# Optimization experiments

Hardware: AMD Instinct MI355X
Metric: run time of the kernel (lower is better)

The kernel has to match this reference:

```python
import jax, jax.numpy as jnp
import numpy as np

TEMP = 0.1
EDGE_THR = 0.25
PATCH = 16
SAMPLE = 100
EPS = 1e-12


def _split_into_patches(feats, P):
    # replicates torch unfold(2).unfold(3).unfold(4).contiguous().view(B,-1,C,P,P,P)
    B, C, D, H, W = feats.shape
    x = feats.reshape(B, C, D // P, P, H // P, P, W // P, P)
    x = x.transpose(0, 1, 2, 4, 6, 3, 5, 7)  # [B,C,Dp,Hp,Wp,P,P,P]
    return x.reshape(B, -1, C, P, P, P)       # C-order reshape == torch .view on contiguous


def _projector(x, w1, b1, w2, b2):
    # torch Linear: y = x @ W.T + b
    h = jax.nn.relu(jnp.matmul(x, w1.T) + b1)
    return jnp.matmul(h, w2.T) + b2


def _normalize(x, axis):
    n = jnp.sqrt(jnp.sum(x * x, axis=axis, keepdims=True))
    return x / jnp.maximum(n, EPS)


def _conv3d(x, w, b, padding):
    y = jax.lax.conv_general_dilated(
        x, w, window_strides=(1, 1, 1), padding=padding,
        dimension_numbers=('NCDHW', 'OIDHW', 'NCDHW'))
    return y + b[None, :, None, None, None]


def setup_inputs() -> dict:
    key = jax.random.key(0)
    ks = jax.random.split(key, 12)
    B, C, D, H, W = 2, 128, 64, 64, 64
    inp = {
        'anchor_feats': jax.random.normal(ks[0], (B, C, D, H, W), dtype=jnp.float32),
        'positive_feats': jax.random.normal(ks[1], (B, C, D, H, W), dtype=jnp.float32),
        'conv1_w': jax.random.normal(ks[2], (32, C, 3, 3, 3), dtype=jnp.float32) * 0.02,
        'conv1_b': jnp.zeros((32,), dtype=jnp.float32),
        'conv2_w': jax.random.normal(ks[3], (1, 32, 1, 1, 1), dtype=jnp.float32) * 0.1,
        'conv2_b': jnp.zeros((1,), dtype=jnp.float32),
        'proj_w1': jax.random.normal(ks[4], (C, C), dtype=jnp.float32) * (1.0 / np.sqrt(C)),
        'proj_b1': jnp.zeros((C,), dtype=jnp.float32),
        'proj_w2': jax.random.normal(ks[5], (64, C), dtype=jnp.float32) * (1.0 / np.sqrt(C)),
        'proj_b2': jnp.zeros((64,), dtype=jnp.float32),
        'loss_weights': jnp.array([1.0, 0.7], dtype=jnp.float32),
        'voxel_idx': jax.random.permutation(ks[6], PATCH ** 3)[:SAMPLE].astype(jnp.int64),
    }
    return inp


def reference(anchor_feats, positive_feats, conv1_w, conv1_b, conv2_w, conv2_b,
              proj_w1, proj_b1, proj_w2, proj_b2, loss_weights, voxel_idx):
    B, C, D, H, W = anchor_feats.shape
    P = PATCH

    # region classifier: Conv3d(C,32,3,p=1) -> ReLU -> Conv3d(32,1,1) -> Sigmoid
    h = jax.nn.relu(_conv3d(anchor_feats, conv1_w, conv1_b, ((1, 1), (1, 1), (1, 1))))
    region_probs = jax.nn.sigmoid(_conv3d(h, conv2_w, conv2_b, ((0, 0), (0, 0), (0, 0))))
    region_mask = (region_probs > EDGE_THR).astype(jnp.float32)  # [B,1,D,H,W]

    anchor_p = _split_into_patches(anchor_feats, P)    # [B,N,C,P,P,P]
    positive_p = _split_into_patches(positive_feats, P)
    region_p = _split_into_patches(region_mask, P)     # [B,N,1,P,P,P]

    edge_ratio = jnp.mean(region_p, axis=(2, 3, 4, 5))  # [B,N]
    mask_vox = (edge_ratio > 0.6).astype(jnp.float32)
    mask_patch = (edge_ratio < 0.4).astype(jnp.float32)

    # ---- patch-level contrast (vectorized over B,N) ----
    a_vec = jnp.mean(anchor_p, axis=(3, 4, 5))    # [B,N,C]
    p_vec = jnp.mean(positive_p, axis=(3, 4, 5))
    a_proj = _normalize(_projector(a_vec, proj_w1, proj_b1, proj_w2, proj_b2), -1)
    p_proj = _normalize(_projector(p_vec, proj_w1, proj_b1, proj_w2, proj_b2), -1)
    patch_losses = -jnp.sum(a_proj * p_proj, axis=-1) / TEMP  # [B,N]

    # ---- voxel-level contrast (vectorized over B,N) ----
    N = anchor_p.shape[1]
    a_vox = anchor_p.reshape(B, N, C, P ** 3).transpose(0, 1, 3, 2)[:, :, voxel_idx, :]  # [B,N,S,C]
    p_vox = positive_p.reshape(B, N, C, P ** 3).transpose(0, 1, 3, 2)[:, :, voxel_idx, :]
    a_vp = _normalize(_projector(a_vox, proj_w1, proj_b1, proj_w2, proj_b2), -1)  # [B,N,S,64]
    p_vp = _normalize(_projector(p_vox, proj_w1, proj_b1, proj_w2, proj_b2), -1)
    sim = jnp.einsum('bnsd,bntd->bnst', a_vp, p_vp) / TEMP  # [B,N,S,S]
    lse = jax.nn.logsumexp(sim, axis=-1)                    # [B,N,S]
    diag = jnp.diagonal(sim, axis1=-2, axis2=-1)            # [B,N,S]
    vox_losses = jnp.mean(lse - diag, axis=-1)              # [B,N]

    patch_sum = jnp.sum(patch_losses * mask_patch)
    vox_sum = jnp.sum(vox_losses * mask_vox)
    valid = jnp.sum(mask_patch) + jnp.sum(mask_vox)

    total = (loss_weights[0] * patch_sum + loss_weights[1] * vox_sum)
    return jnp.where(valid > 0, total / jnp.maximum(valid, 1.0), 0.0)
```

## Files before the change

### kernel.cpp

```cpp
#include <hip/hip_runtime.h>

using short8 = __attribute__((ext_vector_type(8))) short;
using f32x16 = __attribute__((ext_vector_type(16))) float;

#define THR_LOGIT (-1.0986122886681098f)
#define ZPAGE_OFF 156509184

__device__ __forceinline__ unsigned short f2bf(float f) {
  unsigned u = __float_as_uint(f);
  u = (u + 0x7FFFu + ((u >> 16) & 1u)) >> 16;
  return (unsigned short)u;
}

__device__ __forceinline__ void async_copy16(void* lds, const void* g) {
  __builtin_amdgcn_global_load_lds(
      (const __attribute__((address_space(1))) unsigned int*)g,
      (__attribute__((address_space(3))) unsigned int*)lds, 16, 0, 0);
}

__global__ void __launch_bounds__(256) k_prep(const float* __restrict__ c1w,
    const float* __restrict__ pw1, const float* __restrict__ pw2,
    short* __restrict__ wt2, float* __restrict__ w1t, float* __restrict__ w2t) {
  int i = blockIdx.x * 256 + threadIdx.x;
  if (i < 110592) {
    int j8 = i & 7, l31v = (i >> 3) & 31, halfv = (i >> 8) & 1;
    int q = i >> 9;
    int dz = q % 3; q /= 3;
    int dx = q % 3; q /= 3;
    int dy = q % 3; int co8 = q / 3;
    int c = co8 * 16 + halfv * 8 + j8;
    int tap = dz * 9 + dy * 3 + dx;
    wt2[i] = (short)f2bf(c1w[l31v * 3456 + c * 27 + tap]);
  } else if (i < 126976) {
    int i2 = i - 110592; int c = i2 >> 7; int j = i2 & 127;
    w1t[i2] = pw1[j * 128 + c];
  } else if (i < 135168) {
    int i3 = i - 126976; int j = i3 >> 6; int d = i3 & 63;
    w2t[i3] = pw2[d * 128 + j];
  }
}

__global__ void k_inv(const int* __restrict__ vidx, int* __restrict__ inv) {
  int t = threadIdx.x;
  for (int k = t; k < 4096; k += 256) inv[k] = -1;
  __syncthreads();
  if (t < 100) inv[vidx[t]] = t;
}

__global__ void __launch_bounds__(256) k_stage(const float* __restrict__ src,
    short* __restrict__ in2, float* __restrict__ S4, float* __restrict__ Xmat,
    const int* __restrict__ inv, int vox_row_base) {
  __shared__ float tile[128][65];
  __shared__ int mcnt;
  __shared__ int mx[64];
  __shared__ int mrow[64];
  int bi = blockIdx.x;
  int b = bi >> 8, z = (bi >> 2) & 63, yp = bi & 3;
  int t = threadIdx.x;
  int zp = z >> 4, pz = z & 15;
  int cc = t & 127, xh = t >> 7;
  float part0 = 0.f, part1 = 0.f;

  for (int y0 = 0; y0 < 16; ++y0) {
    int y = yp * 16 + y0;
    __syncthreads();
    if (t == 0) mcnt = 0;
    {
      int xq = (t & 15) * 4, w = t >> 4;
      const float* sp = src + (long)b * 128 * 262144 + (long)z * 4096 + (long)y * 64 + xq;
      #pragma unroll
      for (int s = 0; s < 8; ++s) {
        int c = s * 16 + w;
        float4 v = *(const float4*)(sp + (long)c * 262144);
        tile[c][xq + 0] = v.x;
        tile[c][xq + 1] = v.y;
        tile[c][xq + 2] = v.z;
        tile[c][xq + 3] = v.w;
      }
    }
    __syncthreads();
    if (in2 != nullptr) {
      long rowbase = ((long)(b * 64 + z) * 64 + y) * 8192;
      int x = t >> 2, q = t & 3;
      int slot = (q & 1) ^ ((x >> 2) & 1);
      #pragma unroll
      for (int i = 0; i < 4; ++i) {
        int co8 = i * 2 + (q >> 1);
        short8 pk;
        #pragma unroll
        for (int j = 0; j < 8; ++j) pk[j] = (short)f2bf(tile[i * 32 + q * 8 + j][x]);
        *(short8*)(in2 + rowbase + co8 * 1024 + x * 16 + slot * 8) = pk;
      }
    }
    {
      float s0 = 0.f, s1 = 0.f;
      #pragma unroll
      for (int px = 0; px < 16; ++px) s0 += tile[cc][(xh * 2) * 16 + px];
      #pragma unroll
      for (int px = 0; px < 16; ++px) s1 += tile[cc][(xh * 2 + 1) * 16 + px];
      part0 += s0; part1 += s1;
    }
    if (t < 64) {
      int s = inv[pz * 256 + y0 * 16 + (t & 15)];
      if (s >= 0) {
        int idx = atomicAdd(&mcnt, 1);
        mx[idx] = t;
        int n = zp * 16 + yp * 4 + (t >> 4);
        mrow[idx] = vox_row_base + (b * 64 + n) * 100 + s;
      }
    }
    __syncthreads();
    int mc = mcnt;
    for (int i = 0; i < mc; ++i) {
      if (t < 128) Xmat[(long)mrow[i] * 128 + t] = tile[t][mx[i]];
    }
  }
  long sb = ((long)(b * 64 + z) * 4 + yp) * 512;
  S4[sb + cc * 4 + xh * 2 + 0] = part0;
  S4[sb + cc * 4 + xh * 2 + 1] = part1;
}

__global__ void __launch_bounds__(256, 2) k_conv(const short* __restrict__ in2,
    const short* __restrict__ wt2, const float* __restrict__ c1b,
    const float* __restrict__ c2w, const float* __restrict__ c2b,
    int* __restrict__ counts) {
  extern __shared__ char smem[];
  __shared__ int lcnt[4];
  int bi0 = blockIdx.x;
  int bi = ((bi0 & 7) << 7) | (bi0 >> 3);
  int b = bi >> 9, zb = (bi >> 4) & 31, yg = bi & 15;
  int z0 = zb * 2, y0 = yg * 4;
  int tid = threadIdx.x;
  int lane = tid & 63;
  int l31 = lane & 31, half = lane >> 5;
  int wave = tid >> 6;
  int xh = wave & 1, yo = wave >> 1;

  if (tid < 4) lcnt[tid] = 0;
  *(int*)(smem + 49152 + tid * 4) = 0;
  int zoff = 49152 + lane * 16;

  int gbase[12];
  int gmask[12];
  #pragma unroll
  for (int k = 0; k < 12; ++k) {
    int g = k * 256 + tid;
    int row = g >> 7, pos = g & 127;
    int zz = z0 - 1 + row / 6;
    int yy = y0 - 1 + row % 6;
    bool v = ((unsigned)zz < 64u) && ((unsigned)yy < 64u);
    gbase[k] = v ? (((b * 64 + zz) * 64 + yy) * 16384 + pos * 16)
                 : (ZPAGE_OFF + pos * 16);
    gmask[k] = v ? -1 : 0;
  }
  const char* gsrc = (const char*)in2;

  int xbase = xh * 32 + l31;
  int offA[3];
  int vmA[3];
  #pragma unroll
  for (int d = 0; d < 3; ++d) {
    int xp = xbase + d - 1;
    bool v = (unsigned)xp < 64u;
    int xc = min(max(xp, 0), 63);
    offA[d] = v ? (xc * 32 + ((half ^ ((xc >> 2) & 1)) << 4)) : zoff;
    vmA[d] = v ? -1 : 0;
  }
  int ybase = yo * 4096;
  const short8* pBbase = (const short8*)wt2 + half * 32 + l31;

  f32x16 acc[2][2] = {};

  #pragma unroll
  for (int k = 0; k < 12; ++k)
    async_copy16(smem + (k * 256 + tid) * 16, gsrc + gbase[k]);
  __syncthreads();

  for (int co8 = 0; co8 < 8; ++co8) {
    #pragma unroll
    for (int dx = 0; dx < 3; ++dx) {
      int m = vmA[dx], o = offA[dx];
      short8 A[4][4];
      #pragma unroll
      for (int zs = 0; zs < 4; ++zs)
        #pragma unroll
        for (int yr = 0; yr < 4; ++yr)
          A[zs][yr] = *(const short8*)(smem +
              (((zs * 12288 + yr * 2048) + ybase) & m) + o);
      __builtin_amdgcn_s_setprio(1);
      #pragma unroll
      for (int dz = 0; dz < 3; ++dz) {
        #pragma unroll
        for (int dy = 0; dy < 3; ++dy) {
          short8 bf = pBbase[((co8 * 9 + dy * 3 + dx) * 3 + dz) * 64];
          acc[0][0] = __builtin_amdgcn_mfma_f32_32x32x16_bf16(A[dz + 0][dy + 0], bf, acc[0][0], 0, 0, 0);
          acc[1][0] = __builtin_amdgcn_mfma_f32_32x32x16_bf16(A[dz + 1][dy + 0], bf, acc[1][0], 0, 0, 0);
          acc[0][1] = __builtin_amdgcn_mfma_f32_32x32x16_bf16(A[dz + 0][dy + 1], bf, acc[0][1], 0, 0, 0);
          acc[1][1] = __builtin_amdgcn_mfma_f32_32x32x16_bf16(A[dz + 1][dy + 1], bf, acc[1][1], 0, 0, 0);
        }
      }
      __builtin_amdgcn_s_setprio(0);
    }
    __syncthreads();
    if (co8 < 7) {
      int cadd = (co8 + 1) * 2048;
      #pragma unroll
      for (int k = 0; k < 12; ++k)
        async_copy16(smem + (k * 256 + tid) * 16,
                     gsrc + gbase[k] + (cadd & gmask[k]));
      __syncthreads();
    }
  }

  float b1v = c1b[l31];
  float w2v = c2w[l31];
  float b2v = c2b[0];
  int cnt0 = 0, cnt1 = 0;
  #pragma unroll
  for (int zi = 0; zi < 2; ++zi) {
    #pragma unroll
    for (int yi = 0; yi < 2; ++yi) {
      #pragma unroll
      for (int r = 0; r < 16; ++r) {
        float v = fmaxf(acc[zi][yi][r] + b1v, 0.f) * w2v;
        v += __shfl_xor(v, 1);
        v += __shfl_xor(v, 2);
        v += __shfl_xor(v, 4);
        v += __shfl_xor(v, 8);
        v += __shfl_xor(v, 16);
        int bit = (v + b2v) > THR_LOGIT;
        if (r < 8) cnt0 += bit; else cnt1 += bit;
      }
    }
  }
  if (l31 == 0) {
    atomicAdd(&lcnt[xh * 2 + 0], cnt0);
    atomicAdd(&lcnt[xh * 2 + 1], cnt1);
  }
  __syncthreads();
  if (tid < 4) {
    int n = (zb >> 3) * 16 + (yg >> 2) * 4 + tid;
    atomicAdd(&counts[b * 64 + n], lcnt[tid]);
  }
}

__global__ void __launch_bounds__(256) k_vecreduce(const float* __restrict__ S4a,
    const float* __restrict__ S4p, float* __restrict__ Xmat) {
  int g = blockIdx.x * 256 + threadIdx.x;
  int ten = g >> 14, rem = g & 16383;
  int b = rem >> 13, n = (rem >> 7) & 63, c = rem & 127;
  int zp = n >> 4, yp = (n >> 2) & 3, xp = n & 3;
  const float* S = ten ? S4p : S4a;
  float s = 0.f;
  #pragma unroll
  for (int k = 0; k < 16; ++k)
    s += S[((long)(b * 64 + zp * 16 + k) * 4 + yp) * 512 + c * 4 + xp];
  Xmat[(long)(ten * 128 + b * 64 + n) * 128 + c] = s * (1.f / 4096.f);
}

__global__ void __launch_bounds__(256) k_proj(const float* __restrict__ Xmat,
    const float* __restrict__ w1t, const float* __restrict__ pb1,
    const float* __restrict__ w2t, const float* __restrict__ pb2,
    float* __restrict__ P) {
  __shared__ float xsT[128][20];
  __shared__ float hsT[128][20];
  __shared__ float os[16][68];
  int bi = blockIdx.x;
  long row0 = (long)bi * 16;
  int t = threadIdx.x;
  {
    int r = t >> 4, c0 = (t & 15) * 8;
    const float* xp = Xmat + (row0 + r) * 128 + c0;
    #pragma unroll
    for (int k = 0; k < 8; ++k) xsT[c0 + k][r] = xp[k];
  }
  __syncthreads();
  {
    int j = t & 127, rh = t >> 7;
    float hacc[8];
    float bb = pb1[j];
    #pragma unroll
    for (int r8 = 0; r8 < 8; ++r8) hacc[r8] = bb;
    for (int c = 0; c < 128; ++c) {
      float w = w1t[c * 128 + j];
      float4 xlo = *(const float4*)&xsT[c][rh * 8];
      float4 xhi = *(const float4*)&xsT[c][rh * 8 + 4];
      hacc[0] += xlo.x * w; hacc[1] += xlo.y * w; hacc[2] += xlo.z * w; hacc[3] += xlo.w * w;
      hacc[4] += xhi.x * w; hacc[5] += xhi.y * w; hacc[6] += xhi.z * w; hacc[7] += xhi.w * w;
    }
    #pragma unroll
    for (int r8 = 0; r8 < 8; ++r8) hsT[j][rh * 8 + r8] = fmaxf(hacc[r8], 0.f);
  }
  __syncthreads();
  {
    int d = t & 63, rq = t >> 6;
    float oacc[4];
    float bb = pb2[d];
    #pragma unroll
    for (int r4 = 0; r4 < 4; ++r4) oacc[r4] = bb;
    for (int j = 0; j < 128; ++j) {
      float w = w2t[j * 64 + d];
      float4 hv = *(const float4*)&hsT[j][rq * 4];
      oacc[0] += hv.x * w; oacc[1] += hv.y * w; oacc[2] += hv.z * w; oacc[3] += hv.w * w;
    }
    #pragma unroll
    for (int r4 = 0; r4 < 4; ++r4) os[rq * 4 + r4][d] = oacc[r4];
  }
  __syncthreads();
  {
    int r = t >> 4, dg = t & 15;
    float4 v = *(const float4*)&os[r][dg * 4];
    float ss = v.x * v.x + v.y * v.y + v.z * v.z + v.w * v.w;
    ss += __shfl_xor(ss, 1); ss += __shfl_xor(ss, 2);
    ss += __shfl_xor(ss, 4); ss += __shfl_xor(ss, 8);
    float sc = 1.f / fmaxf(sqrtf(ss), 1e-12f);
    float4 o; o.x = v.x * sc; o.y = v.y * sc; o.z = v.z * sc; o.w = v.w * sc;
    *(float4*)&P[(row0 + r) * 64 + dg * 4] = o;
  }
}

__global__ void __launch_bounds__(128) k_sim(const float* __restrict__ P,
                                             float* __restrict__ vloss) {
  __shared__ float ps[100][68];
  __shared__ float red[128];
  int bn = blockIdx.x;
  int t = threadIdx.x;
  long pbase = (long)(13056 + bn * 100) * 64;
  for (int i = t; i < 1600; i += 128) {
    int r = i >> 4, dg = i & 15;
    *(float4*)&ps[r][dg * 4] = *(const float4*)&P[pbase + r * 64 + dg * 4];
  }
  float4 areg[16];
  long abase = (long)(256 + bn * 100) * 64;
  if (t < 100) {
    #pragma unroll
    for (int j = 0; j < 16; ++j) areg[j] = *(const float4*)&P[abase + (long)t * 64 + j * 4];
  }
  __syncthreads();
  float res = 0.f;
  if (t < 100) {
    float m = -1e30f, sum = 0.f, diag = 0.f;
    for (int t2 = 0; t2 < 100; ++t2) {
      float d = 0.f;
      #pragma unroll
      for (int j = 0; j < 16; ++j) {
        float4 pv = *(const float4*)&ps[t2][j * 4];
        d += areg[j].x * pv.x + areg[j].y * pv.y + areg[j].z * pv.z + areg[j].w * pv.w;
      }
      float sim = d * 10.f;
      if (t2 == t) diag = sim;
      float nm = fmaxf(m, sim);
      sum = sum * __expf(m - nm) + __expf(sim - nm);
      m = nm;
    }
    res = m + logf(sum) - diag;
  }
  red[t] = res;
  __syncthreads();
  if (t == 0) {
    float s = 0.f;
    for (int i = 0; i < 100; ++i) s += red[i];
    vloss[bn] = s * 0.01f;
  }
}

__global__ void __launch_bounds__(128) k_final(const float* __restrict__ P,
    const float* __restrict__ vloss, const int* __restrict__ counts,
    const float* __restrict__ lw, float* __restrict__ out) {
  int t = threadIdx.x;
  int lane = t & 63;
  float pterm = 0.f, vterm = 0.f; int vcnt = 0;
  {
    int c = counts[t];
    bool maskv = c >= 2458;
    bool maskp = c <= 1638;
    float d = 0.f;
    for (int k = 0; k < 64; ++k) d += P[t * 64 + k] * P[(128 + t) * 64 + k];
    if (maskp) { pterm = -d * 10.f; vcnt += 1; }
    if (maskv) { vterm = vloss[t];  vcnt += 1; }
  }
  for (int m = 1; m < 64; m <<= 1) {
    pterm += __shfl_xor(pterm, m);
    vterm += __shfl_xor(vterm, m);
    vcnt  += __shfl_xor(vcnt, m);
  }
  __shared__ float sp[2], sv[2]; __shared__ int sc[2];
  if (lane == 0) { sp[t >> 6] = pterm; sv[t >> 6] = vterm; sc[t >> 6] = vcnt; }
  __syncthreads();
  if (t == 0) {
    float psum = sp[0] + sp[1], vsum = sv[0] + sv[1];
    int vc = sc[0] + sc[1];
    float total = lw[0] * psum + lw[1] * vsum;
    out[0] = (vc > 0) ? total / (float)vc : 0.f;
  }
}

extern "C" void kernel_launch(void* const* d_in, const int* in_sizes, int n_in,
                              void* d_out, int out_size, void* d_ws, size_t ws_size,
                              hipStream_t stream) {
  const float* anchor   = (const float*)d_in[0];
  const float* positive = (const float*)d_in[1];
  const float* c1w = (const float*)d_in[2];
  const float* c1b = (const float*)d_in[3];
  const float* c2w = (const float*)d_in[4];
  const float* c2b = (const float*)d_in[5];
  const float* pw1 = (const float*)d_in[6];
  const float* pb1 = (const float*)d_in[7];
  const float* pw2 = (const float*)d_in[8];
  const float* pb2 = (const float*)d_in[9];
  const float* lw  = (const float*)d_in[10];
  const int*   vidx = (const int*)d_in[11];

  char* ws = (char*)d_ws;
  short* in2   = (short*)(ws + 0);
  float* S4a   = (float*)(ws + 134217728);
  float* S4p   = (float*)(ws + 135266304);
  float* X     = (float*)(ws + 136314880);
  float* P     = (float*)(ws + 149553152);
  short* wt2   = (short*)(ws + 156172288);
  float* w1t   = (float*)(ws + 156393472);
  float* w2t   = (float*)(ws + 156459008);
  int*   inv   = (int*)  (ws + 156491776);
  int*   counts= (int*)  (ws + 156508160);
  float* vloss = (float*)(ws + 156508672);
  short* zpage = (short*)(ws + ZPAGE_OFF);

  hipFuncSetAttribute(reinterpret_cast<const void*>(k_conv),
                      hipFuncAttributeMaxDynamicSharedMemorySize, 50176);

  hipMemsetAsync(counts, 0, 128 * sizeof(int), stream);
  hipMemsetAsync(zpage, 0, 16384, stream);
  k_prep<<<528, 256, 0, stream>>>(c1w, pw1, pw2, wt2, w1t, w2t);
  k_inv<<<1, 256, 0, stream>>>(vidx, inv);
  k_stage<<<512, 256, 0, stream>>>(anchor,   in2,     S4a, X, inv, 256);
  k_stage<<<512, 256, 0, stream>>>(positive, nullptr, S4p, X, inv, 13056);
  k_conv<<<1024, 256, 50176, stream>>>(in2, wt2, c1b, c2w, c2b, counts);
  k_vecreduce<<<128, 256, 0, stream>>>(S4a, S4p, X);
  k_proj<<<1616, 256, 0, stream>>>(X, w1t, pb1, w2t, pb2, P);
  k_sim<<<128, 128, 0, stream>>>(P, vloss);
  k_final<<<1, 128, 0, stream>>>(P, vloss, counts, lw, (float*)d_out);
}
```

Before: 415.2 us.

## Fuse positive-feature staging into conv kernel as interleaved block role

```diff
diff --git a/kernel.cpp b/kernel.cpp
--- a/kernel.cpp
+++ b/kernel.cpp
@@ -47,6 +47,74 @@
   if (t < 100) inv[vidx[t]] = t;
 }
 
+__device__ __forceinline__ void stage_body(float (*tile)[65], int* mcnt_p, int* mx,
+    int* mrow, int bi, int t, const float* __restrict__ src, short* __restrict__ in2,
+    float* __restrict__ S4, float* __restrict__ Xmat, const int* __restrict__ inv,
+    int vox_row_base) {
+  int b = bi >> 8, z = (bi >> 2) & 63, yp = bi & 3;
+  int zp = z >> 4, pz = z & 15;
+  int cc = t & 127, xh = t >> 7;
+  float part0 = 0.f, part1 = 0.f;
+
+  for (int y0 = 0; y0 < 16; ++y0) {
+    int y = yp * 16 + y0;
+    __syncthreads();
+    if (t == 0) *mcnt_p = 0;
+    {
+      int xq = (t & 15) * 4, w = t >> 4;
+      const float* sp = src + (long)b * 128 * 262144 + (long)z * 4096 + (long)y * 64 + xq;
+      #pragma unroll
+      for (int s = 0; s < 8; ++s) {
+        int c = s * 16 + w;
+        float4 v = *(const float4*)(sp + (long)c * 262144);
+        tile[c][xq + 0] = v.x;
+        tile[c][xq + 1] = v.y;
+        tile[c][xq + 2] = v.z;
+        tile[c][xq + 3] = v.w;
+      }
+    }
+    __syncthreads();
+    if (in2 != nullptr) {
+      long rowbase = ((long)(b * 64 + z) * 64 + y) * 8192;
+      int x = t >> 2, q = t & 3;
+      int slot = (q & 1) ^ ((x >> 2) & 1);
+      #pragma unroll
+      for (int i = 0; i < 4; ++i) {
+        int co8 = i * 2 + (q >> 1);
+        short8 pk;
+        #pragma unroll
+        for (int j = 0; j < 8; ++j) pk[j] = (short)f2bf(tile[i * 32 + q * 8 + j][x]);
+        *(short8*)(in2 + rowbase + co8 * 1024 + x * 16 + slot * 8) = pk;
+      }
+    }
+    {
+      float s0 = 0.f, s1 = 0.f;
+      #pragma unroll
+      for (int px = 0; px < 16; ++px) s0 += tile[cc][(xh * 2) * 16 + px];
+      #pragma unroll
+      for (int px = 0; px < 16; ++px) s1 += tile[cc][(xh * 2 + 1) * 16 + px];
+      part0 += s0; part1 += s1;
+    }
+    if (t < 64) {
+      int s = inv[pz * 256 + y0 * 16 + (t & 15)];
+      if (s >= 0) {
+        int idx = atomicAdd(mcnt_p, 1);
+        mx[idx] = t;
+        int n = zp * 16 + yp * 4 + (t >> 4);
+        mrow[idx] = vox_row_base + (b * 64 + n) * 100 + s;
+      }
+    }
+    __syncthreads();
+    int mc = *mcnt_p;
+    for (int i = 0; i < mc; ++i) {
+      if (t < 128) Xmat[(long)mrow[i] * 128 + t] = tile[t][mx[i]];
+    }
+  }
+  long sb = ((long)(b * 64 + z) * 4 + yp) * 512;
+  S4[sb + cc * 4 + xh * 2 + 0] = part0;
+  S4[sb + cc * 4 + xh * 2 + 1] = part1;
+}
+
 __global__ void __launch_bounds__(256) k_stage(const float* __restrict__ src,
     short* __restrict__ in2, float* __restrict__ S4, float* __restrict__ Xmat,
     const int* __restrict__ inv, int vox_row_base) {
@@ -54,83 +122,34 @@
   __shared__ int mcnt;
   __shared__ int mx[64];
   __shared__ int mrow[64];
-  int bi = blockIdx.x;
-  int b = bi >> 8, z = (bi >> 2) & 63, yp = bi & 3;
-  int t = threadIdx.x;
-  int zp = z >> 4, pz = z & 15;
-  int cc = t & 127, xh = t >> 7;
-  float part0 = 0.f, part1 = 0.f;
-
-  for (int y0 = 0; y0 < 16; ++y0) {
-    int y = yp * 16 + y0;
-    __syncthreads();
-    if (t == 0) mcnt = 0;
-    {
-      int xq = (t & 15) * 4, w = t >> 4;
-      const float* sp = src + (long)b * 128 * 262144 + (long)z * 4096 + (long)y * 64 + xq;
-      #pragma unroll
-      for (int s = 0; s < 8; ++s) {
-        int c = s * 16 + w;
-        float4 v = *(const float4*)(sp + (long)c * 262144);
-        tile[c][xq + 0] = v.x;
-        tile[c][xq + 1] = v.y;
-        tile[c][xq + 2] = v.z;
-        tile[c][xq + 3] = v.w;
-      }
-    }
-    __syncthreads();
-    if (in2 != nullptr) {
-      long rowbase = ((long)(b * 64 + z) * 64 + y) * 8192;
-      int x = t >> 2, q = t & 3;
-      int slot = (q & 1) ^ ((x >> 2) & 1);
-      #pragma unroll
-      for (int i = 0; i < 4; ++i) {
-        int co8 = i * 2 + (q >> 1);
-        short8 pk;
-        #pragma unroll
-        for (int j = 0; j < 8; ++j) pk[j] = (short)f2bf(tile[i * 32 + q * 8 + j][x]);
-        *(short8*)(in2 + rowbase + co8 * 1024 + x * 16 + slot * 8) = pk;
-      }
-    }
-    {
-      float s0 = 0.f, s1 = 0.f;
-      #pragma unroll
-      for (int px = 0; px < 16; ++px) s0 += tile[cc][(xh * 2) * 16 + px];
-      #pragma unroll
-      for (int px = 0; px < 16; ++px) s1 += tile[cc][(xh * 2 + 1) * 16 + px];
-      part0 += s0; part1 += s1;
-    }
-    if (t < 64) {
-      int s = inv[pz * 256 + y0 * 16 + (t & 15)];
-      if (s >= 0) {
-        int idx = atomicAdd(&mcnt, 1);
-        mx[idx] = t;
-        int n = zp * 16 + yp * 4 + (t >> 4);
-        mrow[idx] = vox_row_base + (b * 64 + n) * 100 + s;
-      }
-    }
-    __syncthreads();
-    int mc = mcnt;
-    for (int i = 0; i < mc; ++i) {
-      if (t < 128) Xmat[(long)mrow[i] * 128 + t] = tile[t][mx[i]];
-    }
-  }
-  long sb = ((long)(b * 64 + z) * 4 + yp) * 512;
-  S4[sb + cc * 4 + xh * 2 + 0] = part0;
-  S4[sb + cc * 4 + xh * 2 + 1] = part1;
-}
-
-__global__ void __launch_bounds__(256, 2) k_conv(const short* __restrict__ in2,
+  stage_body(tile, &mcnt, mx, mrow, blockIdx.x, threadIdx.x,
+             src, in2, S4, Xmat, inv, vox_row_base);
+}
+
+__global__ void __launch_bounds__(256, 2) k_fused(const short* __restrict__ in2,
     const short* __restrict__ wt2, const float* __restrict__ c1b,
     const float* __restrict__ c2w, const float* __restrict__ c2b,
-    int* __restrict__ counts) {
+    int* __restrict__ counts,
+    const float* __restrict__ positive, float* __restrict__ S4p,
+    float* __restrict__ Xmat, const int* __restrict__ inv) {
   extern __shared__ char smem[];
   __shared__ int lcnt[4];
-  int bi0 = blockIdx.x;
+  __shared__ int mx[64];
+  __shared__ int mrow[64];
+  int bid = blockIdx.x;
+  int role = bid % 3;
+  int tid = threadIdx.x;
+
+  if (role == 2) {
+    stage_body((float(*)[65])smem, &lcnt[0], mx, mrow, bid / 3, tid,
+               positive, nullptr, S4p, Xmat, inv, 13056);
+    return;
+  }
+
+  int bi0 = (bid / 3) * 2 + role;
   int bi = ((bi0 & 7) << 7) | (bi0 >> 3);
   int b = bi >> 9, zb = (bi >> 4) & 31, yg = bi & 15;
   int z0 = zb * 2, y0 = yg * 4;
-  int tid = threadIdx.x;
   int lane = tid & 63;
   int l31 = lane & 31, half = lane >> 5;
   int wave = tid >> 6;
@@ -425,16 +444,16 @@
   float* vloss = (float*)(ws + 156508672);
   short* zpage = (short*)(ws + ZPAGE_OFF);
 
-  hipFuncSetAttribute(reinterpret_cast<const void*>(k_conv),
+  hipFuncSetAttribute(reinterpret_cast<const void*>(k_fused),
                       hipFuncAttributeMaxDynamicSharedMemorySize, 50176);
 
   hipMemsetAsync(counts, 0, 128 * sizeof(int), stream);
   hipMemsetAsync(zpage, 0, 16384, stream);
   k_prep<<<528, 256, 0, stream>>>(c1w, pw1, pw2, wt2, w1t, w2t);
   k_inv<<<1, 256, 0, stream>>>(vidx, inv);
-  k_stage<<<512, 256, 0, stream>>>(anchor,   in2,     S4a, X, inv, 256);
-  k_stage<<<512, 256, 0, stream>>>(positive, nullptr, S4p, X, inv, 13056);
-  k_conv<<<1024, 256, 50176, stream>>>(in2, wt2, c1b, c2w, c2b, counts);
+  k_stage<<<512, 256, 0, stream>>>(anchor, in2, S4a, X, inv, 256);
+  k_fused<<<1536, 256, 50176, stream>>>(in2, wt2, c1b, c2w, c2b, counts,
+                                        positive, S4p, X, inv);
   k_vecreduce<<<128, 256, 0, stream>>>(S4a, S4p, X);
   k_proj<<<1616, 256, 0, stream>>>(X, w1t, pb1, w2t, pb2, P);
   k_sim<<<128, 128, 0, stream>>>(P, vloss);
```

After: 386.8 us. 1.07x faster.
